# Performance work log

Hardware: AMD Instinct MI355X
Metric: run time of the kernel (lower is better)

Reference implementation:

```python
import jax, jax.numpy as jnp
import numpy as np

N = 8192
M = 16
F_NODE = 128
HID = 512


def setup_inputs() -> dict:
    key = jax.random.key(0)
    ks = jax.random.split(key, 10)
    node_in_fea = jax.random.normal(ks[0], (N, F_NODE), dtype=jnp.float32)
    edge_fea_idx = jax.random.randint(ks[1], (N, M), 0, N, dtype=jnp.int64)
    s_emb = 1.0 / np.sqrt(F_NODE)
    s_h = 1.0 / np.sqrt(HID)
    W_emb = jax.random.uniform(ks[2], (F_NODE, HID), jnp.float32, -s_emb, s_emb)
    b_emb = jax.random.uniform(ks[3], (HID,), jnp.float32, -s_emb, s_emb)
    W1 = jax.random.uniform(ks[4], (HID, HID), jnp.float32, -s_h, s_h)
    b1 = jax.random.uniform(ks[5], (HID,), jnp.float32, -s_h, s_h)
    W2 = jax.random.uniform(ks[6], (HID, HID), jnp.float32, -s_h, s_h)
    b2 = jax.random.uniform(ks[7], (HID,), jnp.float32, -s_h, s_h)
    W3 = jax.random.uniform(ks[8], (HID, HID), jnp.float32, -s_h, s_h)
    b3 = jax.random.uniform(ks[9], (HID,), jnp.float32, -s_h, s_h)
    return {"node_in_fea": node_in_fea, "edge_fea_idx": edge_fea_idx,
            "W_emb": W_emb, "b_emb": b_emb, "W1": W1, "b1": b1,
            "W2": W2, "b2": b2, "W3": W3, "b3": b3}


def _normalized_adj(edge_fea_idx, n):
    # build dense adjacency: adj[i, j] += 1 for each valid neighbor j of i
    rows = jnp.broadcast_to(jnp.arange(n)[:, None], edge_fea_idx.shape)
    valid = edge_fea_idx >= 0  # -1 marks invalid neighbor
    cols = jnp.where(valid, edge_fea_idx, 0)
    vals = valid.astype(jnp.float32)
    adj = jnp.zeros((n, n), jnp.float32).at[rows.reshape(-1), cols.reshape(-1)].add(vals.reshape(-1))
    # add self-loops, symmetric normalization D^{-1/2} A D^{-1/2}
    adj = adj + jnp.eye(n, dtype=jnp.float32)
    deg = jnp.sum(adj, axis=1)
    d_inv_sqrt = jnp.where(deg > 0, deg ** -0.5, 0.0)
    return adj * d_inv_sqrt[:, None] * d_inv_sqrt[None, :]


def reference(node_in_fea, edge_fea_idx, W_emb, b_emb, W1, b1, W2, b2, W3, b3):
    adj = _normalized_adj(edge_fea_idx, node_in_fea.shape[0])
    x = node_in_fea @ W_emb + b_emb          # (N, HID)
    x = jax.nn.relu((adj @ x) @ W1 + b1)     # gcn1 + relu
    x = jax.nn.relu((adj @ x) @ W2 + b2)     # gcn2 + relu
    x = (adj @ x) @ W3 + b3                  # gcn3 (no relu)
    return x
```

## Files before the change

### kernel.cpp

```cpp
#include <hip/hip_runtime.h>
#include <stdint.h>

#define NN 8192
#define MM 16
#define FN 128
#define HH 512

typedef unsigned short u16;
typedef unsigned int u32;
typedef __bf16 bf16;
typedef __bf16 bf16x8 __attribute__((ext_vector_type(8)));
typedef float f32x4 __attribute__((ext_vector_type(4)));

__device__ __forceinline__ void gld_lds16(const u16* g, u16* l) {
  __builtin_amdgcn_global_load_lds(
      (const __attribute__((address_space(1))) void*)g,
      (__attribute__((address_space(3))) void*)l, 16, 0, 0);
}

__device__ __forceinline__ int probe_f32(const u16* w) {
  int lane = threadIdx.x & 63;
  int e = (w[2 * lane] >> 7) & 0xFF;
  unsigned long long m = __ballot(!(e == 0 || (e >= 90 && e <= 140)));
  return __popcll(m) >= 8;
}
__device__ __forceinline__ int probe_i64(const u32* w) {
  int lane = threadIdx.x & 63;
  unsigned long long m = __ballot(lane < 32 && w[2 * lane + 1] != 0);
  return m == 0;
}
__device__ __forceinline__ bf16 cvt_elem(const void* p, size_t i, int f32) {
  return f32 ? (bf16)((const float*)p)[i] : ((const bf16*)p)[i];
}

__device__ __forceinline__ void transpose_tile(const void* __restrict__ W,
                                               u16* __restrict__ T, int tt,
                                               int f32in, u16* sm) {
  const int k0 = (tt >> 4) * 32, n0 = (tt & 15) * 32;
  const int tx = threadIdx.x & 31, ty = threadIdx.x >> 5;
#pragma unroll
  for (int r = ty; r < 32; r += 8) {
    bf16 v = cvt_elem(W, (size_t)(k0 + r) * HH + n0 + tx, f32in);
    sm[r * 33 + tx] = *(u16*)&v;
  }
  __syncthreads();
#pragma unroll
  for (int r = ty; r < 32; r += 8)
    T[(size_t)(n0 + r) * HH + k0 + tx] = sm[tx * 33 + r];
}

__device__ __forceinline__ void gemm_tile(const void* __restrict__ A, int K,
                                          int af32, const u16* __restrict__ Bt,
                                          const float* __restrict__ biasf,
                                          int rtile, int ctile,
                                          u16* __restrict__ C, int cstride,
                                          u16* As, u16* Bs) {
  const int tid = threadIdx.x;
  const int wave = tid >> 6, lane = tid & 63;
  const int wr = wave >> 1, wc = wave & 1;
  const int quad = lane >> 4, l16 = lane & 15;
  f32x4 acc[2][4] = {};

  int arow[2], agc[2], brow[4], bgc[4];
#pragma unroll
  for (int i = 0; i < 2; ++i) {
    int c = i * 256 + tid;
    arow[i] = c >> 3;
    agc[i] = (c & 7) ^ (arow[i] & 7);
  }
#pragma unroll
  for (int i = 0; i < 4; ++i) {
    int c = i * 256 + tid;
    brow[i] = c >> 3;
    bgc[i] = (c & 7) ^ (brow[i] & 7);
  }
  u16* AsW = As + wave * 512;
  u16* BsW = Bs + wave * 512;

  for (int k0 = 0; k0 < K; k0 += 64) {
    __syncthreads();
    if (af32) {
      const float* Af = (const float*)A;
      bf16x8 v[2];
#pragma unroll
      for (int i = 0; i < 2; ++i) {
        const float* p = &Af[(size_t)(rtile * 64 + arow[i]) * K + k0 + agc[i] * 8];
        f32x4 x0 = *(const f32x4*)p, x1 = *(const f32x4*)(p + 4);
#pragma unroll
        for (int t = 0; t < 4; ++t) {
          v[i][t] = (bf16)x0[t];
          v[i][4 + t] = (bf16)x1[t];
        }
      }
#pragma unroll
      for (int i = 0; i < 2; ++i) *(bf16x8*)&As[(i * 256 + tid) * 8] = v[i];
    } else {
      const u16* Ab = (const u16*)A;
#pragma unroll
      for (int i = 0; i < 2; ++i)
        gld_lds16(&Ab[(size_t)(rtile * 64 + arow[i]) * K + k0 + agc[i] * 8],
                  AsW + i * 2048);
    }
#pragma unroll
    for (int i = 0; i < 4; ++i)
      gld_lds16(&Bt[(size_t)(ctile * 128 + brow[i]) * K + k0 + bgc[i] * 8],
                BsW + i * 2048);
    __syncthreads();
#pragma unroll
    for (int h = 0; h < 2; ++h) {
      bf16x8 af[2], bfr[4];
#pragma unroll
      for (int i = 0; i < 2; ++i) {
        int r = wr * 32 + i * 16 + l16;
        int cc = (h * 4 + quad) ^ (r & 7);
        af[i] = *(const bf16x8*)&As[r * 64 + cc * 8];
      }
#pragma unroll
      for (int j = 0; j < 4; ++j) {
        int n = wc * 64 + j * 16 + l16;
        int cc = (h * 4 + quad) ^ (n & 7);
        bfr[j] = *(const bf16x8*)&Bs[n * 64 + cc * 8];
      }
#pragma unroll
      for (int i = 0; i < 2; ++i)
#pragma unroll
        for (int j = 0; j < 4; ++j)
          acc[i][j] = __builtin_amdgcn_mfma_f32_16x16x32_bf16(af[i], bfr[j],
                                                              acc[i][j], 0, 0, 0);
    }
  }

  const int crow0 = rtile * 64 + wr * 32 + quad * 4;
  const int ccol0 = ctile * 128 + wc * 64 + l16;
#pragma unroll
  for (int j = 0; j < 4; ++j) {
    const int col = ccol0 + j * 16;
    const float bv = biasf ? biasf[col] : 0.f;
#pragma unroll
    for (int i = 0; i < 2; ++i)
#pragma unroll
      for (int r = 0; r < 4; ++r) {
        bf16 o = (bf16)(acc[i][j][r] + bv);
        C[(size_t)(crow0 + i * 16 + r) * cstride + col] = *(u16*)&o;
      }
  }
}

__device__ void wc_tile(int vb, const void* __restrict__ Wemb,
                        const void* __restrict__ W1, int f32in,
                        u16* __restrict__ TWc, u16* As, u16* Bs) {
  const int tid = threadIdx.x;
  const int rtile = vb >> 2, ctile = vb & 3;
  const int wave = tid >> 6, lane = tid & 63;
  const int wr = wave >> 1, wc = wave & 1;
  const int quad = lane >> 4, l16 = lane & 15;
  f32x4 acc[2][4] = {};
  int arow[2], agc[2];
#pragma unroll
  for (int i = 0; i < 2; ++i) {
    int c = i * 256 + tid;
    arow[i] = c >> 3;
    agc[i] = (c & 7) ^ (arow[i] & 7);
  }
  for (int k0 = 0; k0 < HH; k0 += 64) {
    __syncthreads();
#pragma unroll
    for (int i = 0; i < 2; ++i) {
      size_t src = (size_t)(rtile * 64 + arow[i]) * HH + k0 + agc[i] * 8;
      bf16x8 av;
      if (f32in) {
        const float* pp = (const float*)Wemb + src;
        f32x4 x0 = *(const f32x4*)pp, x1 = *(const f32x4*)(pp + 4);
#pragma unroll
        for (int t = 0; t < 4; ++t) { av[t] = (bf16)x0[t]; av[4 + t] = (bf16)x1[t]; }
      } else {
        av = *(const bf16x8*)((const u16*)Wemb + src);
      }
      *(bf16x8*)&As[(i * 256 + tid) * 8] = av;
    }
#pragma unroll
    for (int i = 0; i < 4; ++i) {
      int t2 = i * 256 + tid;
      int kk = t2 >> 4, seg = (t2 & 15) * 8;
      size_t src = (size_t)(k0 + kk) * HH + ctile * 128 + seg;
      bf16 e8[8];
      if (f32in) {
        const float* pp = (const float*)W1 + src;
        f32x4 x0 = *(const f32x4*)pp, x1 = *(const f32x4*)(pp + 4);
#pragma unroll
        for (int t = 0; t < 4; ++t) { e8[t] = (bf16)x0[t]; e8[4 + t] = (bf16)x1[t]; }
      } else {
        bf16x8 v = *(const bf16x8*)((const u16*)W1 + src);
#pragma unroll
        for (int t = 0; t < 8; ++t) e8[t] = v[t];
      }
#pragma unroll
      for (int j = 0; j < 8; ++j) {
        int n = seg + j;
        int cc = (kk >> 3) ^ j;
        Bs[n * 64 + cc * 8 + (kk & 7)] = *(u16*)&e8[j];
      }
    }
    __syncthreads();
#pragma unroll
    for (int h = 0; h < 2; ++h) {
      bf16x8 af[2], bfr[4];
#pragma unroll
      for (int i = 0; i < 2; ++i) {
        int r = wr * 32 + i * 16 + l16;
        int cc = (h * 4 + quad) ^ (r & 7);
        af[i] = *(const bf16x8*)&As[r * 64 + cc * 8];
      }
#pragma unroll
      for (int j = 0; j < 4; ++j) {
        int n = wc * 64 + j * 16 + l16;
        int cc = (h * 4 + quad) ^ (n & 7);
        bfr[j] = *(const bf16x8*)&Bs[n * 64 + cc * 8];
      }
#pragma unroll
      for (int i = 0; i < 2; ++i)
#pragma unroll
        for (int j = 0; j < 4; ++j)
          acc[i][j] = __builtin_amdgcn_mfma_f32_16x16x32_bf16(af[i], bfr[j],
                                                              acc[i][j], 0, 0, 0);
    }
  }
  const int crow0 = rtile * 64 + wr * 32 + quad * 4;
  const int ccol0 = ctile * 128 + wc * 64 + l16;
#pragma unroll
  for (int j = 0; j < 4; ++j)
#pragma unroll
    for (int i = 0; i < 2; ++i)
#pragma unroll
      for (int r = 0; r < 4; ++r) {
        bf16 o = (bf16)acc[i][j][r];
        TWc[(size_t)(ccol0 + j * 16) * FN + crow0 + i * 16 + r] = *(u16*)&o;
      }
}

__global__ __launch_bounds__(256) void prep_kernel(
    const u16* __restrict__ node, const u32* __restrict__ idxw,
    const void* __restrict__ Wemb, const void* __restrict__ bemb,
    const void* __restrict__ W1, const void* __restrict__ W2,
    float* __restrict__ dis, float* __restrict__ bvec, u16* __restrict__ TWc,
    u16* __restrict__ TW2) {
  __shared__ __align__(16) u16 smem[12288];
  const int bid = blockIdx.x, tid = threadIdx.x;
  const int f32in = probe_f32(node);
  if (bid < 256) {
    transpose_tile(W2, TW2, bid, f32in, smem);
  } else if (bid < 288) {
    const int i64 = probe_i64(idxw);
    const int* idx = (const int*)idxw;
    const int i = (bid - 256) * 256 + tid;
    int c = 1;
#pragma unroll
    for (int e = 0; e < MM; ++e) c += (idx[(i * MM + e) << i64] >= 0) ? 1 : 0;
    dis[i] = rsqrtf((float)c);
  } else if (bid < 296) {
    wc_tile(bid - 288, Wemb, W1, f32in, TWc, smem, smem + 4096);
  } else {
    float* bembS = (float*)smem;
    bembS[tid] = (float)cvt_elem(bemb, tid, f32in);
    bembS[256 + tid] = (float)cvt_elem(bemb, 256 + tid, f32in);
    __syncthreads();
    const int n = (bid - 296) * 256 + tid;
    float acc = 0.f;
    if (f32in) {
      const float* W1f = (const float*)W1;
#pragma unroll 16
      for (int m = 0; m < HH; ++m) acc += bembS[m] * W1f[(size_t)m * HH + n];
    } else {
      const u16* W1b = (const u16*)W1;
#pragma unroll 16
      for (int m = 0; m < HH; ++m)
        acc += bembS[m] * (float)(*(const bf16*)&W1b[(size_t)m * HH + n]);
    }
    bvec[n] = acc;
  }
}

__global__ __launch_bounds__(256) void g1_kernel(const u16* __restrict__ node,
                                                 const void* __restrict__ W3,
                                                 const u16* __restrict__ TWc,
                                                 const float* __restrict__ bvec,
                                                 u16* __restrict__ TW3,
                                                 u16* __restrict__ C) {
  __shared__ __align__(16) u16 smem[12288];
  const int bid = blockIdx.x;
  const int f32in = probe_f32(node);
  if (bid < 512) {
    gemm_tile(node, FN, f32in, TWc, bvec, bid >> 2, bid & 3, C, HH, smem,
              smem + 4096);
  } else {
    transpose_tile(W3, TW3, bid - 512, f32in, smem);
  }
}

__global__ __launch_bounds__(256) void gemm_mid(const u16* __restrict__ A,
                                                const u16* __restrict__ Bt,
                                                u16* __restrict__ C) {
  __shared__ __align__(16) u16 smem[12288];
  gemm_tile(A, HH, 0, Bt, nullptr, blockIdx.x, blockIdx.y, C, HH, smem,
            smem + 4096);
}

template <bool RELU, bool FINAL>
__global__ __launch_bounds__(256) void agg_kernel(
    const u16* __restrict__ t, const u32* __restrict__ idxw,
    const float* __restrict__ dis, const void* __restrict__ bias,
    const u16* __restrict__ nodeprobe, void* __restrict__ y) {
  const int i64 = probe_i64(idxw);
  const int f32io = probe_f32(nodeprobe);
  const int* idx = (const int*)idxw;
  const int b = blockIdx.x;
  const int strip = (b & 7) >> 1;
  const int grp = (b >> 3) * 2 + (b & 1);
  const int wave = threadIdx.x >> 6, lane = threadIdx.x & 63;
  const int node = grp * 16 + wave * 4 + (lane >> 4);
  const int c0 = strip * 128 + (lane & 15) * 8;
  const float wi = dis[node];
  float acc[8];
  bf16x8 xs = *(const bf16x8*)&t[(size_t)node * HH + c0];
#pragma unroll
  for (int k = 0; k < 8; ++k) acc[k] = wi * wi * (float)xs[k];
#pragma unroll
  for (int e = 0; e < MM; ++e) {
    const int j = idx[(node * MM + e) << i64];
    if (j >= 0) {
      const float w = wi * dis[j];
      bf16x8 v = *(const bf16x8*)&t[(size_t)j * HH + c0];
#pragma unroll
      for (int k = 0; k < 8; ++k) acc[k] += w * (float)v[k];
    }
  }
  float bv[8];
  if (f32io) {
    f32x4 b0 = *(const f32x4*)&((const float*)bias)[c0];
    f32x4 b1 = *(const f32x4*)&((const float*)bias)[c0 + 4];
#pragma unroll
    for (int k = 0; k < 4; ++k) { bv[k] = b0[k]; bv[4 + k] = b1[k]; }
  } else {
    bf16x8 bb = *(const bf16x8*)&((const u16*)bias)[c0];
#pragma unroll
    for (int k = 0; k < 8; ++k) bv[k] = (float)bb[k];
  }
#pragma unroll
  for (int k = 0; k < 8; ++k) {
    acc[k] += bv[k];
    if (RELU) acc[k] = fmaxf(acc[k], 0.f);
  }
  if (FINAL && f32io) {
    float* O = (float*)y;
    f32x4 o0, o1;
#pragma unroll
    for (int k = 0; k < 4; ++k) { o0[k] = acc[k]; o1[k] = acc[4 + k]; }
    *(f32x4*)&O[(size_t)node * HH + c0] = o0;
    *(f32x4*)&O[(size_t)node * HH + c0 + 4] = o1;
  } else {
    bf16x8 o;
#pragma unroll
    for (int k = 0; k < 8; ++k) o[k] = (bf16)acc[k];
    *(bf16x8*)&((u16*)y)[(size_t)node * HH + c0] = o;
  }
}

extern "C" void kernel_launch(void* const* d_in, const int* in_sizes, int n_in,
                              void* d_out, int out_size, void* d_ws, size_t ws_size,
                              hipStream_t stream) {
  const u16* node = (const u16*)d_in[0];
  const u32* idxw = (const u32*)d_in[1];
  const void* Wemb = d_in[2];
  const void* bemb = d_in[3];
  const void* W1 = d_in[4];
  const void* b1 = d_in[5];
  const void* W2 = d_in[6];
  const void* b2 = d_in[7];
  const void* W3 = d_in[8];
  const void* b3 = d_in[9];

  char* p = (char*)d_ws;
  float* dis = (float*)p;   p += NN * sizeof(float);
  float* bvec = (float*)p;  p += HH * sizeof(float);
  u16* TWc = (u16*)p;       p += (size_t)HH * FN * 2;
  u16* TW2 = (u16*)p;       p += (size_t)HH * HH * 2;
  u16* TW3 = (u16*)p;       p += (size_t)HH * HH * 2;
  u16* xA = (u16*)p;
  u16* xO = (u16*)d_out;

  prep_kernel<<<298, 256, 0, stream>>>(node, idxw, Wemb, bemb, W1, W2, dis,
                                       bvec, TWc, TW2);
  g1_kernel<<<768, 256, 0, stream>>>(node, W3, TWc, bvec, TW3, xA);
  agg_kernel<true, false>
      <<<NN / 4, 256, 0, stream>>>(xA, idxw, dis, b1, node, xO);
  gemm_mid<<<dim3(128, 4), 256, 0, stream>>>(xO, TW2, xA);
  agg_kernel<true, false>
      <<<NN / 4, 256, 0, stream>>>(xA, idxw, dis, b2, node, xO);
  gemm_mid<<<dim3(128, 4), 256, 0, stream>>>(xO, TW3, xA);
  agg_kernel<false, true>
      <<<NN / 4, 256, 0, stream>>>(xA, idxw, dis, b3, node, d_out);
}
```

Before: 179.4 us.

## Fuse neighbor aggregation with following GEMM into one kernel per layer

Replaces the separate aggregation kernel and the mid GEMM with a fused kernel. Each block aggregates 16 rows into swizzled LDS with bias and ReLU applied, then multiplies them by the transposed weight using MFMA, streaming weight tiles from global memory. This removes two launches and the round trip of the intermediate activations through global memory. In exchange, only 512 blocks run, each computing a 16-row tile, so every block re-reads the full weight matrix, MFMA utilisation per block is low, and output is stored as scalar u16 writes.

```diff
diff --git a/kernel.cpp b/kernel.cpp
--- a/kernel.cpp
+++ b/kernel.cpp
@@ -297,16 +297,107 @@
   }
 }
 
-__global__ __launch_bounds__(256) void gemm_mid(const u16* __restrict__ A,
-                                                const u16* __restrict__ Bt,
-                                                u16* __restrict__ C) {
-  __shared__ __align__(16) u16 smem[12288];
-  gemm_tile(A, HH, 0, Bt, nullptr, blockIdx.x, blockIdx.y, C, HH, smem,
-            smem + 4096);
-}
-
-template <bool RELU, bool FINAL>
-__global__ __launch_bounds__(256) void agg_kernel(
+__global__ __launch_bounds__(256) void ag_kernel(
+    const u16* __restrict__ t, const u32* __restrict__ idxw,
+    const float* __restrict__ dis, const void* __restrict__ bias,
+    const u16* __restrict__ nodeprobe, const u16* __restrict__ Bt,
+    u16* __restrict__ C) {
+  __shared__ __align__(16) u16 Ax[8 * 16 * 64];
+  __shared__ __align__(16) u16 Bs[128 * 64];
+  const int i64 = probe_i64(idxw);
+  const int f32io = probe_f32(nodeprobe);
+  const int* idx = (const int*)idxw;
+  const int bt = blockIdx.x;
+  const int tid = threadIdx.x;
+  const int wave = tid >> 6, lane = tid & 63;
+  const int quad = lane >> 4, l16 = lane & 15;
+
+  for (int pass = 0; pass < 4; ++pass) {
+    const int u = pass * 16 + wave * 4 + (lane >> 4);
+    const int rl = u >> 2, strip = u & 3;
+    const int row = bt * 16 + rl;
+    const int c0 = strip * 128 + l16 * 8;
+    const float wi = dis[row];
+    float acc[8];
+    bf16x8 xs = *(const bf16x8*)&t[(size_t)row * HH + c0];
+#pragma unroll
+    for (int k = 0; k < 8; ++k) acc[k] = wi * wi * (float)xs[k];
+#pragma unroll
+    for (int e = 0; e < MM; ++e) {
+      const int j = idx[(row * MM + e) << i64];
+      if (j >= 0) {
+        const float w = wi * dis[j];
+        bf16x8 v = *(const bf16x8*)&t[(size_t)j * HH + c0];
+#pragma unroll
+        for (int k = 0; k < 8; ++k) acc[k] += w * (float)v[k];
+      }
+    }
+    float bv[8];
+    if (f32io) {
+      f32x4 b0 = *(const f32x4*)&((const float*)bias)[c0];
+      f32x4 b1 = *(const f32x4*)&((const float*)bias)[c0 + 4];
+#pragma unroll
+      for (int k = 0; k < 4; ++k) { bv[k] = b0[k]; bv[4 + k] = b1[k]; }
+    } else {
+      bf16x8 bb = *(const bf16x8*)&((const u16*)bias)[c0];
+#pragma unroll
+      for (int k = 0; k < 8; ++k) bv[k] = (float)bb[k];
+    }
+    bf16x8 o;
+#pragma unroll
+    for (int k = 0; k < 8; ++k) o[k] = (bf16)fmaxf(acc[k] + bv[k], 0.f);
+    const int gc = strip * 16 + l16;
+    const int kb = gc >> 3;
+    const int cc = (gc & 7) ^ (rl & 7);
+    *(bf16x8*)&Ax[(kb * 16 + rl) * 64 + cc * 8] = o;
+  }
+
+  u16* BsW = Bs + wave * 512;
+  for (int ctile = 0; ctile < 4; ++ctile) {
+    f32x4 acc2[2] = {};
+    for (int kb = 0; kb < 8; ++kb) {
+      __syncthreads();
+#pragma unroll
+      for (int i = 0; i < 4; ++i) {
+        int c = i * 256 + tid;
+        int brow = c >> 3;
+        int bgc = (c & 7) ^ (brow & 7);
+        gld_lds16(&Bt[(size_t)(ctile * 128 + brow) * HH + kb * 64 + bgc * 8],
+                  BsW + i * 2048);
+      }
+      __syncthreads();
+#pragma unroll
+      for (int h = 0; h < 2; ++h) {
+        bf16x8 af, bfr[2];
+        {
+          int cc = (h * 4 + quad) ^ (l16 & 7);
+          af = *(const bf16x8*)&Ax[(kb * 16 + l16) * 64 + cc * 8];
+        }
+#pragma unroll
+        for (int j = 0; j < 2; ++j) {
+          int n = wave * 32 + j * 16 + l16;
+          int cc = (h * 4 + quad) ^ (n & 7);
+          bfr[j] = *(const bf16x8*)&Bs[n * 64 + cc * 8];
+        }
+#pragma unroll
+        for (int j = 0; j < 2; ++j)
+          acc2[j] = __builtin_amdgcn_mfma_f32_16x16x32_bf16(af, bfr[j], acc2[j],
+                                                            0, 0, 0);
+      }
+    }
+    const int crow0 = bt * 16 + quad * 4;
+    const int ccol0 = ctile * 128 + wave * 32 + l16;
+#pragma unroll
+    for (int j = 0; j < 2; ++j)
+#pragma unroll
+      for (int r = 0; r < 4; ++r) {
+        bf16 o = (bf16)acc2[j][r];
+        C[(size_t)(crow0 + r) * HH + ccol0 + j * 16] = *(u16*)&o;
+      }
+  }
+}
+
+__global__ __launch_bounds__(256) void agg_final(
     const u16* __restrict__ t, const u32* __restrict__ idxw,
     const float* __restrict__ dis, const void* __restrict__ bias,
     const u16* __restrict__ nodeprobe, void* __restrict__ y) {
@@ -346,11 +437,8 @@
     for (int k = 0; k < 8; ++k) bv[k] = (float)bb[k];
   }
 #pragma unroll
-  for (int k = 0; k < 8; ++k) {
-    acc[k] += bv[k];
-    if (RELU) acc[k] = fmaxf(acc[k], 0.f);
-  }
-  if (FINAL && f32io) {
+  for (int k = 0; k < 8; ++k) acc[k] += bv[k];
+  if (f32io) {
     float* O = (float*)y;
     f32x4 o0, o1;
 #pragma unroll
@@ -391,12 +479,7 @@
   prep_kernel<<<298, 256, 0, stream>>>(node, idxw, Wemb, bemb, W1, W2, dis,
                                        bvec, TWc, TW2);
   g1_kernel<<<768, 256, 0, stream>>>(node, W3, TWc, bvec, TW3, xA);
-  agg_kernel<true, false>
-      <<<NN / 4, 256, 0, stream>>>(xA, idxw, dis, b1, node, xO);
-  gemm_mid<<<dim3(128, 4), 256, 0, stream>>>(xO, TW2, xA);
-  agg_kernel<true, false>
-      <<<NN / 4, 256, 0, stream>>>(xA, idxw, dis, b2, node, xO);
-  gemm_mid<<<dim3(128, 4), 256, 0, stream>>>(xO, TW3, xA);
-  agg_kernel<false, true>
-      <<<NN / 4, 256, 0, stream>>>(xA, idxw, dis, b3, node, d_out);
-}
+  ag_kernel<<<512, 256, 0, stream>>>(xA, idxw, dis, b1, node, TW2, xO);
+  ag_kernel<<<512, 256, 0, stream>>>(xO, idxw, dis, b2, node, TW3, xA);
+  agg_final<<<NN / 4, 256, 0, stream>>>(xA, idxw, dis, b3, node, d_out);
+}
```

New measurement: 245.0 us. 36.6% more time.
